# Optimization experiments

Measured on AMD Instinct MI355X. Metric: run time of the kernel, lower is better.

The kernel has to match this reference:

```python
import jax, jax.numpy as jnp
import numpy as np

N = 16384  # n_nodes
D = 64     # feature dim


def setup_inputs() -> dict:
    key = jax.random.key(0)
    kx, ka = jax.random.split(key)
    x = jax.random.normal(kx, (N, D), dtype=jnp.float32)
    # original code only tests adj[idx] == 1, so 0/1 int entries are faithful
    adj = jax.random.randint(ka, (N, N), 0, 2, dtype=jnp.int32)
    return {"x": x, "adj": adj}


def reference(x, adj):
    # GraphPool: for each node, sum its own feature vector plus the feature
    # vectors of all neighbors j with adj[i, j] == 1.
    # Vectorized: out = adj @ x + x  (dense binary SpMM + self term).
    a = (adj == 1).astype(x.dtype)  # [N, N]
    return jnp.matmul(a, x) + x     # [N, D]
```

## Files before the change

kernel.cpp:

```cpp
#include <hip/hip_runtime.h>

#define NN 16384
#define DD 64

typedef _Float16 f16x8 __attribute__((ext_vector_type(8)));
typedef float    f32x4 __attribute__((ext_vector_type(4)));
typedef int      i32x4 __attribute__((ext_vector_type(4)));

__device__ __forceinline__ int kperm(int q, int j) {
    return q * 4 + (j & 3) + ((j >> 2) << 4);
}

__global__ __launch_bounds__(256) void prep_x(const float* __restrict__ x,
                                              _Float16* __restrict__ ws) {
    int tid = blockIdx.x * 256 + threadIdx.x;
    int l  = tid & 63;
    int tc = tid >> 6;
    int c  = tc & 3;
    int t  = tc >> 2;
    int q  = l >> 4;
    int m  = l & 15;
    int col = c * 16 + m;
    f16x8 v;
#pragma unroll
    for (int j = 0; j < 8; ++j) {
        int row = t * 32 + kperm(q, j);
        v[j] = (_Float16)x[(size_t)row * DD + col];
    }
    *(f16x8*)(ws + (size_t)tid * 8) = v;
}

__global__ __launch_bounds__(64, 2) void graphpool_gemm(const int* __restrict__ adj,
                                                        const float* __restrict__ x,
                                                        const _Float16* __restrict__ xs,
                                                        float* __restrict__ out) {
    const int l = threadIdx.x;
    const int q = l >> 4;
    const int m = l & 15;
    const int row16 = blockIdx.x * 16;

    const int* aptr = adj + (size_t)(row16 + m) * NN + q * 4;
    const f16x8* bbase = (const f16x8*)xs + l;

    f32x4 acc[4];
#pragma unroll
    for (int c = 0; c < 4; ++c) acc[c] = (f32x4){0.f, 0.f, 0.f, 0.f};

    i32x4 areg[2][4][2];
    f16x8 breg[2][16];

    auto loadA = [&](int n, int buf) {
        const int* base = aptr + (size_t)n * 128;
#pragma unroll
        for (int s = 0; s < 4; ++s) {
            areg[buf][s][0] = *(const i32x4*)(base + s * 32);
            areg[buf][s][1] = *(const i32x4*)(base + s * 32 + 16);
        }
    };
    auto loadB = [&](int n, int buf) {
        const f16x8* src = bbase + (size_t)n * 1024;
#pragma unroll
        for (int f = 0; f < 16; ++f) breg[buf][f] = src[f * 64];
    };
    auto compute = [&](int buf) {
#pragma unroll
        for (int s = 0; s < 4; ++s) {
            i32x4 v0 = areg[buf][s][0], v1 = areg[buf][s][1];
            i32x4 p;
            p.x = (v0.x + (v0.y << 16)) * 0x3C00;
            p.y = (v0.z + (v0.w << 16)) * 0x3C00;
            p.z = (v1.x + (v1.y << 16)) * 0x3C00;
            p.w = (v1.z + (v1.w << 16)) * 0x3C00;
            f16x8 af = __builtin_bit_cast(f16x8, p);
#pragma unroll
            for (int c = 0; c < 4; ++c)
                acc[c] = __builtin_amdgcn_mfma_f32_16x16x32_f16(af, breg[buf][s * 4 + c],
                                                                acc[c], 0, 0, 0);
        }
    };

    loadB(0, 0);
    loadA(0, 0);

    for (int n = 0; n < NN / 128; n += 2) {
        if (n + 1 < NN / 128) { loadB(n + 1, 1); loadA(n + 1, 1); }
        compute(0);
        if (n + 2 < NN / 128) { loadB(n + 2, 0); loadA(n + 2, 0); }
        compute(1);
    }

#pragma unroll
    for (int c = 0; c < 4; ++c) {
#pragma unroll
        for (int r = 0; r < 4; ++r) {
            int row = row16 + q * 4 + r;
            int col = c * 16 + m;
            size_t off = (size_t)row * DD + col;
            out[off] = acc[c][r] + x[off];
        }
    }
}

__global__ void graphpool_fallback(const int* __restrict__ adj,
                                   const float* __restrict__ x,
                                   float* __restrict__ out) {
    int i = blockIdx.x;
    int d = threadIdx.x;
    float acc = x[(size_t)i * DD + d];
    const int* row = adj + (size_t)i * NN;
    for (int j = 0; j < NN; ++j)
        if (row[j]) acc += x[(size_t)j * DD + d];
    out[(size_t)i * DD + d] = acc;
}

extern "C" void kernel_launch(void* const* d_in, const int* in_sizes, int n_in,
                              void* d_out, int out_size, void* d_ws, size_t ws_size,
                              hipStream_t stream) {
    const float* x   = (const float*)d_in[0];
    const int*   adj = (const int*)d_in[1];
    float*       out = (float*)d_out;

    const size_t ws_needed = (size_t)NN * DD * sizeof(_Float16);
    if (ws_size >= ws_needed) {
        _Float16* xs = (_Float16*)d_ws;
        prep_x<<<512, 256, 0, stream>>>(x, xs);
        graphpool_gemm<<<NN / 16, 64, 0, stream>>>(adj, x, xs, out);
    } else {
        graphpool_fallback<<<NN, 64, 0, stream>>>(adj, x, out);
    }
}
```

Measured before the change: 1.394 ms.

## Split K across four waves per block with LDS reduction

```diff
diff --git a/kernel.cpp b/kernel.cpp
--- a/kernel.cpp
+++ b/kernel.cpp
@@ -30,41 +30,45 @@
     *(f16x8*)(ws + (size_t)tid * 8) = v;
 }
 
-__global__ __launch_bounds__(64, 2) void graphpool_gemm(const int* __restrict__ adj,
-                                                        const float* __restrict__ x,
-                                                        const _Float16* __restrict__ xs,
-                                                        float* __restrict__ out) {
-    const int l = threadIdx.x;
-    const int q = l >> 4;
-    const int m = l & 15;
+__global__ __launch_bounds__(256, 4) void graphpool_gemm(const int* __restrict__ adj,
+                                                         const float* __restrict__ x,
+                                                         const _Float16* __restrict__ xs,
+                                                         float* __restrict__ out) {
+    __shared__ float red[4 * 1024];
+
+    const int tid = threadIdx.x;
+    const int w   = tid >> 6;
+    const int l   = tid & 63;
+    const int q   = l >> 4;
+    const int m   = l & 15;
     const int row16 = blockIdx.x * 16;
 
-    const int* aptr = adj + (size_t)(row16 + m) * NN + q * 4;
-    const f16x8* bbase = (const f16x8*)xs + l;
+    const int* aptr = adj + (size_t)(row16 + m) * NN + w * 4096 + q * 4;
+    const f16x8* bbase = (const f16x8*)xs + (size_t)w * 128 * 256 + l;
 
     f32x4 acc[4];
 #pragma unroll
     for (int c = 0; c < 4; ++c) acc[c] = (f32x4){0.f, 0.f, 0.f, 0.f};
 
-    i32x4 areg[2][4][2];
-    f16x8 breg[2][16];
+    i32x4 areg[2][2][2];
+    f16x8 breg[8];
 
     auto loadA = [&](int n, int buf) {
-        const int* base = aptr + (size_t)n * 128;
+        const int* base = aptr + n * 64;
 #pragma unroll
-        for (int s = 0; s < 4; ++s) {
+        for (int s = 0; s < 2; ++s) {
             areg[buf][s][0] = *(const i32x4*)(base + s * 32);
             areg[buf][s][1] = *(const i32x4*)(base + s * 32 + 16);
         }
     };
-    auto loadB = [&](int n, int buf) {
-        const f16x8* src = bbase + (size_t)n * 1024;
+    auto loadB = [&](int n) {
+        const f16x8* src = bbase + n * 8 * 64;
 #pragma unroll
-        for (int f = 0; f < 16; ++f) breg[buf][f] = src[f * 64];
+        for (int f = 0; f < 8; ++f) breg[f] = src[f * 64];
     };
     auto compute = [&](int buf) {
 #pragma unroll
-        for (int s = 0; s < 4; ++s) {
+        for (int s = 0; s < 2; ++s) {
             i32x4 v0 = areg[buf][s][0], v1 = areg[buf][s][1];
             i32x4 p;
             p.x = (v0.x + (v0.y << 16)) * 0x3C00;
@@ -74,29 +78,42 @@
             f16x8 af = __builtin_bit_cast(f16x8, p);
 #pragma unroll
             for (int c = 0; c < 4; ++c)
-                acc[c] = __builtin_amdgcn_mfma_f32_16x16x32_f16(af, breg[buf][s * 4 + c],
+                acc[c] = __builtin_amdgcn_mfma_f32_16x16x32_f16(af, breg[s * 4 + c],
                                                                 acc[c], 0, 0, 0);
         }
     };
 
-    loadB(0, 0);
+    loadB(0);
     loadA(0, 0);
-
-    for (int n = 0; n < NN / 128; n += 2) {
-        if (n + 1 < NN / 128) { loadB(n + 1, 1); loadA(n + 1, 1); }
+    for (int n = 0; n < 64; n += 2) {
+        if (n + 1 < 64) loadA(n + 1, 1);
         compute(0);
-        if (n + 2 < NN / 128) { loadB(n + 2, 0); loadA(n + 2, 0); }
+        loadB(n + 1);
+        if (n + 2 < 64) loadA(n + 2, 0);
         compute(1);
+        if (n + 2 < 64) loadB(n + 2);
     }
 
 #pragma unroll
-    for (int c = 0; c < 4; ++c) {
+    for (int c = 0; c < 4; ++c)
 #pragma unroll
-        for (int r = 0; r < 4; ++r) {
-            int row = row16 + q * 4 + r;
-            int col = c * 16 + m;
-            size_t off = (size_t)row * DD + col;
-            out[off] = acc[c][r] + x[off];
+        for (int i = 0; i < 4; ++i)
+            red[w * 1024 + (c * 4 + i) * 64 + l] = acc[c][i];
+    __syncthreads();
+
+    {
+        int col = tid & 63;
+        int g   = tid >> 6;
+        int c   = col >> 4;
+        int mm  = col & 15;
+#pragma unroll
+        for (int rr = 0; rr < 4; ++rr) {
+            int r = rr * 4 + g;
+            float s = x[(size_t)(row16 + r) * DD + col];
+#pragma unroll
+            for (int ww = 0; ww < 4; ++ww)
+                s += red[ww * 1024 + (c * 4 + g) * 64 + rr * 16 + mm];
+            out[(size_t)(row16 + r) * DD + col] = s;
         }
     }
 }
@@ -124,7 +141,7 @@
     if (ws_size >= ws_needed) {
         _Float16* xs = (_Float16*)d_ws;
         prep_x<<<512, 256, 0, stream>>>(x, xs);
-        graphpool_gemm<<<NN / 16, 64, 0, stream>>>(adj, x, xs, out);
+        graphpool_gemm<<<NN / 16, 256, 0, stream>>>(adj, x, xs, out);
     } else {
         graphpool_fallback<<<NN, 64, 0, stream>>>(adj, x, out);
     }
```

After: 1.397 ms. No clear change (+0.2%).
